# Optimization experiments

Measured on AMD Instinct MI355X. Metric: run time of the kernel, lower is better.

Reference implementation:

```python
import jax, jax.numpy as jnp
import numpy as np

EPS = 1e-12

def _l2norm(x):
    # F.normalize(p=2, dim=1) with eps clamp on the norm
    n = jnp.linalg.norm(x, axis=1, keepdims=True)
    return x / jnp.maximum(n, EPS)

def _xavier_uniform(key, shape, gain=1.414):
    fan_in, fan_out = shape[-1], shape[0]
    a = gain * np.sqrt(6.0 / (fan_in + fan_out))
    return jax.random.uniform(key, shape, jnp.float32, -a, a)

def setup_inputs() -> dict:
    NUM_ENT, NUM_REL, D, E, B = 100000, 500, 512, 150000, 4096
    key = jax.random.key(0)
    ks = jax.random.split(key, 12)
    heads = jax.random.randint(ks[0], (B, 1), 0, NUM_ENT)
    rels  = jax.random.randint(ks[1], (B, 1), 0, NUM_REL)
    tails = jax.random.randint(ks[2], (B, 1), 0, NUM_ENT)
    triples = jnp.concatenate([heads, rels, tails], axis=1)           # [B,3]
    node_list = jax.random.randint(ks[3], (2, E), 0, NUM_ENT)          # [2,E] (src,dst)
    edge_list = jax.random.randint(ks[4], (E,), 0, NUM_REL)            # [E] relation per edge
    return {
        "triples": triples,
        "node_list": node_list,
        "edge_list": edge_list,
        "ent_emb_init": jax.random.normal(ks[5], (NUM_ENT, D), jnp.float32),
        "rel_emb_init": jax.random.normal(ks[6], (NUM_REL, D), jnp.float32),
        "W_1": _xavier_uniform(ks[7], (D, D)),
        "W_a": _xavier_uniform(ks[8], (1, D)),
        "g_0": _xavier_uniform(ks[9], (1, D)),
        "W_E": _xavier_uniform(ks[10], (D, D)),
        "W_R": _xavier_uniform(ks[11], (D, D)),
    }

def reference(triples, node_list, edge_list, ent_emb_init, rel_emb_init,
              W_1, W_a, g_0, W_E, W_R):
    num_ent = ent_emb_init.shape[0]
    e0 = _l2norm(ent_emb_init)                      # normalized entity table [N,D]
    src, dst = node_list[0], node_list[1]
    h_i = e0[src]                                   # [E,D]
    h_j = e0[dst]                                   # [E,D]
    g_k = rel_emb_init[edge_list]                   # [E,D]

    # c_ijk = W_1 @ (h_j*g_k)^T  -> kept edge-major as [E,D]
    c = (h_j * g_k) @ W_1.T                         # [E,D]
    a = -jax.nn.leaky_relu((h_i * jnp.tanh(c)) @ W_a[0], 0.2)   # [E]
    c_base = (h_i * g_0) @ W_1.T                    # [E,D]
    a_base = -jax.nn.leaky_relu((h_i * jnp.tanh(c_base)) @ W_a[0], 0.2)  # [E]

    a_exp = jnp.exp(a)                              # [E]
    ab_exp = jnp.exp(a_base)                        # [E]

    # segment-softmax denominator: sum of edge exps per source node + baseline term
    a_exp_sum = jax.ops.segment_sum(a_exp[:, None], src, num_segments=num_ent)  # [N,1]
    # baseline exp depends only on src node -> duplicate scatter-set writes identical values
    ab_sorted = jnp.zeros_like(a_exp_sum).at[src].set(ab_exp[:, None])           # [N,1]
    denom = ab_sorted + a_exp_sum
    denom = jnp.where(denom == 0.0, EPS, denom)

    # weighted scatter-aggregate of messages (dropout omitted: eval-mode identity)
    ac = a_exp[:, None] * c                         # [E,D]
    ac_base = ab_exp[:, None] * c_base              # [E,D]
    a_new = jax.ops.segment_sum(ac, src, num_segments=num_ent)                   # [N,D]
    ab_new = jnp.zeros_like(a_new).at[src].set(ac_base)                          # [N,D]

    h_prime = jax.nn.elu((ab_new + a_new) / denom)  # [N,D]
    ent_new = _l2norm(e0 @ W_E + h_prime)           # [N,D]
    rel_new = rel_emb_init @ W_R                    # [R,D]

    head = ent_new[triples[:, 0]][:, None, :]       # [B,1,D]
    rel  = rel_new[triples[:, 1]][:, None, :]       # [B,1,D]
    tail = ent_new[triples[:, 2]][:, None, :]       # [B,1,D]
    return jnp.concatenate([head, rel, tail], axis=1)  # [B,3,D]
```

## Files before the change

kernel.cpp:

```cpp
#include <hip/hip_runtime.h>
#include <cmath>


#define DDIM 512
#define MAXM 65536
#define GBM 128
#define GBN 128

typedef __attribute__((ext_vector_type(8))) short short8;
typedef __attribute__((ext_vector_type(4))) float fv4;
typedef unsigned short u16;

__device__ __forceinline__ float elu1(float x) { return x > 0.f ? x : expm1f(x); }
__device__ __forceinline__ float sexp(float x) {
    float lr = x >= 0.f ? x : 0.2f * x;
    return expf(-lr);
}
__device__ __forceinline__ u16 f2bf(float x) {
    unsigned u = __float_as_uint(x);
    u += 0x7FFFu + ((u >> 16) & 1u);
    return (u16)(u >> 16);
}
__device__ __forceinline__ float bf2f(u16 h) {
    return __uint_as_float((unsigned)h << 16);
}
__device__ __forceinline__ void cvt8(const float* v, short8& h8, short8& l8) {
    #pragma unroll
    for (int i = 0; i < 8; i++) {
        u16 h = f2bf(v[i]);
        h8[i] = (short)h;
        l8[i] = (short)f2bf(v[i] - bf2f(h));
    }
}

__global__ __launch_bounds__(128)
void invnorm_sel_kernel(const float* __restrict__ emb, const int* __restrict__ slotNode,
                        const int* __restrict__ rowsL, const int* __restrict__ dstIdx,
                        const int* __restrict__ Mdev, int NS, float* __restrict__ invN)
{
    __shared__ float ws2[2];
    int total = NS + min(MAXM, *Mdev);
    int t = threadIdx.x;
    for (int q = blockIdx.x; q < total; q += gridDim.x) {
        int n = (q < NS) ? slotNode[q] : dstIdx[rowsL[q - NS]];
        float4 v = *(const float4*)(emb + (size_t)n * DDIM + t * 4);
        float s = v.x*v.x + v.y*v.y + v.z*v.z + v.w*v.w;
        #pragma unroll
        for (int off = 32; off > 0; off >>= 1) s += __shfl_down(s, off);
        if ((t & 63) == 0) ws2[t >> 6] = s;
        __syncthreads();
        if (t == 0) invN[n] = 1.f / fmaxf(sqrtf(ws2[0] + ws2[1]), 1e-12f);
        __syncthreads();
    }
}

__global__ __launch_bounds__(128)
void l2norm_kernel(float* __restrict__ data)
{
    int r = blockIdx.x, t = threadIdx.x;
    size_t o = (size_t)r * DDIM + t * 4;
    float4 v = *(const float4*)(data + o);
    float s = v.x*v.x + v.y*v.y + v.z*v.z + v.w*v.w;
    #pragma unroll
    for (int off = 32; off > 0; off >>= 1) s += __shfl_down(s, off);
    __shared__ float ws2[2];
    if ((t & 63) == 0) ws2[t >> 6] = s;
    __syncthreads();
    float inv = 1.f / fmaxf(sqrtf(ws2[0] + ws2[1]), 1e-12f);
    *(float4*)(data + o) = make_float4(v.x*inv, v.y*inv, v.z*inv, v.w*inv);
}

__global__ __launch_bounds__(256)
void transpose512_kernel(const float* __restrict__ in, float* __restrict__ out)
{
    __shared__ float tile[32][33];
    int bx = blockIdx.x & 15, by = blockIdx.x >> 4;
    int x = threadIdx.x & 31, y0 = (threadIdx.x >> 5) * 4;
    #pragma unroll
    for (int i = 0; i < 4; i++)
        tile[y0 + i][x] = in[(size_t)(by * 32 + y0 + i) * 512 + bx * 32 + x];
    __syncthreads();
    #pragma unroll
    for (int i = 0; i < 4; i++)
        out[(size_t)(bx * 32 + y0 + i) * 512 + by * 32 + x] = tile[x][y0 + i];
}

__global__ void hist_kernel(const int* __restrict__ src, int* __restrict__ cnt, int E)
{
    int e = blockIdx.x * 256 + threadIdx.x;
    if (e < E) atomicAdd(&cnt[src[e]], 1);
}

__global__ __launch_bounds__(1024)
void scan1_kernel(const int* __restrict__ in, int* __restrict__ out,
                  int* __restrict__ blockTot, int n)
{
    __shared__ int sh[1024];
    int t = threadIdx.x;
    int i = blockIdx.x * 1024 + t;
    int v = (i < n) ? in[i] : 0;
    sh[t] = v;
    __syncthreads();
    for (int off = 1; off < 1024; off <<= 1) {
        int x = (t >= off) ? sh[t - off] : 0;
        __syncthreads();
        sh[t] += x;
        __syncthreads();
    }
    if (i < n) out[i] = sh[t] - v;
    if (t == 1023) blockTot[blockIdx.x] = sh[1023];
}

__global__ __launch_bounds__(1024)
void scan2_kernel(const int* __restrict__ blockTot, int* __restrict__ blockOff,
                  int* __restrict__ outLast, int G)
{
    __shared__ int sh[1024];
    int t = threadIdx.x;
    int v = (t < G) ? blockTot[t] : 0;
    sh[t] = v;
    __syncthreads();
    for (int off = 1; off < 1024; off <<= 1) {
        int x = (t >= off) ? sh[t - off] : 0;
        __syncthreads();
        sh[t] += x;
        __syncthreads();
    }
    if (t < G) blockOff[t] = sh[t] - v;
    if (t == 1023) *outLast = sh[1023];
}

__global__ __launch_bounds__(1024)
void scan3_kernel(int* __restrict__ out, const int* __restrict__ blockOff, int n)
{
    int i = blockIdx.x * 1024 + threadIdx.x;
    if (i < n) out[i] += blockOff[blockIdx.x];
}

__global__ void bucket_kernel(const int* __restrict__ src, int* __restrict__ cursor,
                              int* __restrict__ edge_ids, int E)
{
    int e = blockIdx.x * 256 + threadIdx.x;
    if (e < E) { int p = atomicAdd(&cursor[src[e]], 1); edge_ids[p] = e; }
}

__global__ void slotdeg_kernel(const int* __restrict__ triples, const int* __restrict__ rowSt,
                               int* __restrict__ slotNode, int* __restrict__ deg, int NS)
{
    int r = blockIdx.x * 256 + threadIdx.x;
    if (r < NS) {
        int b = r >> 1, p = (r & 1) * 2;
        int n = triples[b * 3 + p];
        slotNode[r] = n;
        deg[r] = rowSt[n + 1] - rowSt[n];
    }
}

__global__ void fill_rows_kernel(const int* __restrict__ slotNode, const int* __restrict__ rowSt,
                                 const int* __restrict__ edgeIds, const int* __restrict__ slotOff,
                                 int* __restrict__ rows, int* __restrict__ srcL, int NS)
{
    int r = blockIdx.x * 256 + threadIdx.x;
    if (r >= NS) return;
    int n = slotNode[r];
    int gs = rowSt[n], d = rowSt[n + 1] - gs, mo = slotOff[r];
    for (int j = 0; j < d && mo + j < MAXM; j++) {
        rows[mo + j] = edgeIds[gs + j];
        srcL[mo + j] = n;
    }
}

__global__ __launch_bounds__(256)
void afrag_dense_kernel(const float* __restrict__ in, int rows,
                        u16* __restrict__ hi, u16* __restrict__ lo)
{
    int nt = ((rows + 127) >> 7) << 3;
    int wid = threadIdx.x >> 6, lane = threadIdx.x & 63;
    int l15 = lane & 15, seg = (lane >> 4) * 8;
    for (int rt = blockIdx.x * 4 + wid; rt < nt; rt += gridDim.x * 4) {
        int r = min(rt * 16 + l15, rows - 1);
        const float* p = in + (size_t)r * DDIM + seg;
        size_t base = (size_t)rt * 8192 + (size_t)lane * 8;
        #pragma unroll 4
        for (int kt = 0; kt < 16; kt++) {
            float4 x0 = *(const float4*)(p + kt * 32);
            float4 x1 = *(const float4*)(p + kt * 32 + 4);
            float v[8] = {x0.x, x0.y, x0.z, x0.w, x1.x, x1.y, x1.z, x1.w};
            short8 h8, l8; cvt8(v, h8, l8);
            *(short8*)(hi + base + (size_t)kt * 512) = h8;
            *(short8*)(lo + base + (size_t)kt * 512) = l8;
        }
    }
}

__global__ __launch_bounds__(256)
void afrag_edge_kernel(const float* __restrict__ entEmb, const float* __restrict__ invN,
                       const float* __restrict__ relEmb, const int* __restrict__ rowsL,
                       const int* __restrict__ dstIdx, const int* __restrict__ relIdx,
                       const int* __restrict__ Mdev,
                       u16* __restrict__ hi, u16* __restrict__ lo)
{
    int M = max(1, min(MAXM, *Mdev));
    int nt = ((M + 127) >> 7) << 3;
    int wid = threadIdx.x >> 6, lane = threadIdx.x & 63;
    int l15 = lane & 15, seg = (lane >> 4) * 8;
    for (int rt = blockIdx.x * 4 + wid; rt < nt; rt += gridDim.x * 4) {
        int m = min(rt * 16 + l15, M - 1);
        int e = rowsL[m];
        int dn = dstIdx[e], rl = relIdx[e];
        float sc = invN[dn];
        const float* ep = entEmb + (size_t)dn * DDIM + seg;
        const float* rp = relEmb + (size_t)rl * DDIM + seg;
        size_t base = (size_t)rt * 8192 + (size_t)lane * 8;
        #pragma unroll 4
        for (int kt = 0; kt < 16; kt++) {
            float4 x0 = *(const float4*)(ep + kt * 32);
            float4 x1 = *(const float4*)(ep + kt * 32 + 4);
            float4 y0 = *(const float4*)(rp + kt * 32);
            float4 y1 = *(const float4*)(rp + kt * 32 + 4);
            float v[8] = {sc*x0.x*y0.x, sc*x0.y*y0.y, sc*x0.z*y0.z, sc*x0.w*y0.w,
                          sc*x1.x*y1.x, sc*x1.y*y1.y, sc*x1.z*y1.z, sc*x1.w*y1.w};
            short8 h8, l8; cvt8(v, h8, l8);
            *(short8*)(hi + base + (size_t)kt * 512) = h8;
            *(short8*)(lo + base + (size_t)kt * 512) = l8;
        }
    }
}

__global__ __launch_bounds__(256)
void afrag_slot_kernel(const float* __restrict__ entEmb, const float* __restrict__ invN,
                       const float* __restrict__ g0, const int* __restrict__ slotNode,
                       int NS, u16* __restrict__ s1h, u16* __restrict__ s1l,
                       u16* __restrict__ s3h, u16* __restrict__ s3l)
{
    int nt = ((NS + 127) >> 7) << 3;
    int wid = threadIdx.x >> 6, lane = threadIdx.x & 63;
    int l15 = lane & 15, seg = (lane >> 4) * 8;
    for (int rt = blockIdx.x * 4 + wid; rt < nt; rt += gridDim.x * 4) {
        int r = min(rt * 16 + l15, NS - 1);
        int n = slotNode[r];
        float sc = invN[n];
        const float* ep = entEmb + (size_t)n * DDIM + seg;
        const float* gp = g0 + seg;
        size_t base = (size_t)rt * 8192 + (size_t)lane * 8;
        #pragma unroll 2
        for (int kt = 0; kt < 16; kt++) {
            float4 x0 = *(const float4*)(ep + kt * 32);
            float4 x1 = *(const float4*)(ep + kt * 32 + 4);
            float4 y0 = *(const float4*)(gp + kt * 32);
            float4 y1 = *(const float4*)(gp + kt * 32 + 4);
            float v3[8] = {sc*x0.x, sc*x0.y, sc*x0.z, sc*x0.w,
                           sc*x1.x, sc*x1.y, sc*x1.z, sc*x1.w};
            float v1[8] = {v3[0]*y0.x, v3[1]*y0.y, v3[2]*y0.z, v3[3]*y0.w,
                           v3[4]*y1.x, v3[5]*y1.y, v3[6]*y1.z, v3[7]*y1.w};
            short8 h8, l8;
            cvt8(v3, h8, l8);
            *(short8*)(s3h + base + (size_t)kt * 512) = h8;
            *(short8*)(s3l + base + (size_t)kt * 512) = l8;
            cvt8(v1, h8, l8);
            *(short8*)(s1h + base + (size_t)kt * 512) = h8;
            *(short8*)(s1l + base + (size_t)kt * 512) = l8;
        }
    }
}

template<int EPI, bool DEVM>
__global__ __launch_bounds__(256)
void gemm_frag_k(const u16* __restrict__ Ahi, const u16* __restrict__ Alo,
                 const u16* __restrict__ Bhi, const u16* __restrict__ Blo,
                 const float* __restrict__ entEmb, const float* __restrict__ invNorm,
                 const int* __restrict__ srcMap, const float* __restrict__ Wa,
                 float* __restrict__ scoreOut, const float* __restrict__ invDenom,
                 const float* __restrict__ Hadd, float* __restrict__ Cout,
                 int Mhost, const int* __restrict__ Mdev)
{
    int M = DEVM ? max(1, min(MAXM, *Mdev)) : Mhost;
    int lane = threadIdx.x & 63, wid = threadIdx.x >> 6;
    int waveM = wid >> 1, waveN = wid & 1;
    int quad = lane >> 4, l15 = lane & 15;
    int n0 = blockIdx.y * GBN;

    for (int mt = blockIdx.x; mt * GBM < M; mt += gridDim.x) {
        int m0 = mt * GBM;
        const u16 *aHp[4], *aLp[4], *bHp[4], *bLp[4];
        #pragma unroll
        for (int i = 0; i < 4; i++) {
            size_t rt = (size_t)(m0 >> 4) + waveM * 4 + i;
            aHp[i] = Ahi + rt * 8192 + (size_t)lane * 8;
            aLp[i] = Alo + rt * 8192 + (size_t)lane * 8;
            size_t ntb = (size_t)(n0 >> 4) + waveN * 4 + i;
            bHp[i] = Bhi + ntb * 8192 + (size_t)lane * 8;
            bLp[i] = Blo + ntb * 8192 + (size_t)lane * 8;
        }

        fv4 acc[4][4];
        #pragma unroll
        for (int i = 0; i < 4; i++)
            #pragma unroll
            for (int j = 0; j < 4; j++) acc[i][j] = fv4{0.f, 0.f, 0.f, 0.f};

        short8 aH[4], aL[4], bH[4], bL[4];
        #pragma unroll
        for (int i = 0; i < 4; i++) {
            aH[i] = *(const short8*)aHp[i];
            aL[i] = *(const short8*)aLp[i];
            bH[i] = *(const short8*)bHp[i];
            bL[i] = *(const short8*)bLp[i];
        }

        for (int kt = 0; kt < 16; kt++) {
            short8 nAH[4], nAL[4], nBH[4], nBL[4];
            if (kt < 15) {
                size_t o = (size_t)(kt + 1) * 512;
                #pragma unroll
                for (int i = 0; i < 4; i++) {
                    nAH[i] = *(const short8*)(aHp[i] + o);
                    nAL[i] = *(const short8*)(aLp[i] + o);
                    nBH[i] = *(const short8*)(bHp[i] + o);
                    nBL[i] = *(const short8*)(bLp[i] + o);
                }
            }
            #pragma unroll
            for (int i = 0; i < 4; i++)
                #pragma unroll
                for (int j = 0; j < 4; j++) {
                    acc[i][j] = __builtin_amdgcn_mfma_f32_16x16x32_bf16(aH[i], bH[j], acc[i][j], 0, 0, 0);
                    acc[i][j] = __builtin_amdgcn_mfma_f32_16x16x32_bf16(aH[i], bL[j], acc[i][j], 0, 0, 0);
                    acc[i][j] = __builtin_amdgcn_mfma_f32_16x16x32_bf16(aL[i], bH[j], acc[i][j], 0, 0, 0);
                }
            if (kt < 15) {
                #pragma unroll
                for (int i = 0; i < 4; i++) {
                    aH[i] = nAH[i]; aL[i] = nAL[i];
                    bH[i] = nBH[i]; bL[i] = nBL[i];
                }
            }
        }

        if (EPI == 1) {
            #pragma unroll
            for (int i = 0; i < 4; i++) {
                #pragma unroll
                for (int reg = 0; reg < 4; reg++) {
                    int gm = m0 + waveM * 64 + i * 16 + quad * 4 + reg;
                    bool valid = gm < M;
                    int gmc = valid ? gm : 0;
                    int srcn = srcMap[gmc];
                    float invs = invNorm[srcn];
                    float s = 0.f;
                    #pragma unroll
                    for (int j = 0; j < 4; j++) {
                        int col = n0 + waveN * 64 + j * 16 + l15;
                        float hv = entEmb[(size_t)srcn * DDIM + col];
                        float wv = Wa[col];
                        s += tanhf(acc[i][j][reg]) * hv * wv;
                    }
                    s *= invs;
                    s += __shfl_xor(s, 8); s += __shfl_xor(s, 4);
                    s += __shfl_xor(s, 2); s += __shfl_xor(s, 1);
                    if (l15 == 0 && valid) atomicAdd(scoreOut + gm, s);
                }
            }
        } else {
            #pragma unroll
            for (int i = 0; i < 4; i++) {
                #pragma unroll
                for (int reg = 0; reg < 4; reg++) {
                    int gm = m0 + waveM * 64 + i * 16 + quad * 4 + reg;
                    if (gm >= M) continue;
                    float idv = (EPI == 2) ? invDenom[gm] : 0.f;
                    #pragma unroll
                    for (int j = 0; j < 4; j++) {
                        int col = n0 + waveN * 64 + j * 16 + l15;
                        size_t o = (size_t)gm * DDIM + col;
                        float v = acc[i][j][reg];
                        if (EPI == 2) v = elu1(v * idv);
                        else if (EPI == 3) v += Hadd[o];
                        Cout[o] = v;
                    }
                }
            }
        }
    }
}

__global__ __launch_bounds__(128)
void build_p_kernel(const float* __restrict__ entEmb, const float* __restrict__ invNorm,
                    const float* __restrict__ relEmb, const float* __restrict__ g0,
                    const int* __restrict__ slotNode, const int* __restrict__ rowSt,
                    const int* __restrict__ edgeIds, const int* __restrict__ dstIdx,
                    const int* __restrict__ relIdx, const int* __restrict__ slotOff,
                    const float* __restrict__ scoreE, const float* __restrict__ scoreS,
                    float* __restrict__ P, float* __restrict__ invDenom)
{
    int r = blockIdx.x, t = threadIdx.x;
    int n = slotNode[r];
    int gs = rowSt[n], d = rowSt[n + 1] - gs;
    size_t po = (size_t)r * DDIM + t * 4;
    if (d == 0) {
        *(float4*)(P + po) = make_float4(0.f, 0.f, 0.f, 0.f);
        if (t == 0) invDenom[r] = 1.f;
        return;
    }
    int mo = slotOff[r];
    float ab = sexp(scoreS[r]);
    float sc = ab * invNorm[n];
    float4 ev = *(const float4*)(entEmb + (size_t)n * DDIM + t * 4);
    float4 gv = *(const float4*)(g0 + t * 4);
    float4 acc = make_float4(sc*ev.x*gv.x, sc*ev.y*gv.y, sc*ev.z*gv.z, sc*ev.w*gv.w);
    float denom = ab;
    for (int j = 0; j < d; j++) {
        if (mo + j >= MAXM) break;
        int e = edgeIds[gs + j];
        float ae = sexp(scoreE[mo + j]);
        int dn = dstIdx[e], rl = relIdx[e];
        float s = ae * invNorm[dn];
        float4 dv = *(const float4*)(entEmb + (size_t)dn * DDIM + t * 4);
        float4 rv = *(const float4*)(relEmb + (size_t)rl * DDIM + t * 4);
        acc.x = fmaf(s, dv.x*rv.x, acc.x);
        acc.y = fmaf(s, dv.y*rv.y, acc.y);
        acc.z = fmaf(s, dv.z*rv.z, acc.z);
        acc.w = fmaf(s, dv.w*rv.w, acc.w);
        denom += ae;
    }
    *(float4*)(P + po) = acc;
    if (t == 0) invDenom[r] = 1.f / denom;
}

__global__ __launch_bounds__(128)
void gather_out_kernel(const int* __restrict__ triples, const float* __restrict__ ENT,
                       const float* __restrict__ relnew, float* __restrict__ out)
{
    int r = blockIdx.x;
    int b = r / 3, j = r - b * 3;
    const float* srow;
    if (j == 1) srow = relnew + (size_t)triples[r] * DDIM;
    else        srow = ENT + (size_t)(b * 2 + (j == 2 ? 1 : 0)) * DDIM;
    int t = threadIdx.x * 4;
    *(float4*)(out + (size_t)r * DDIM + t) = *(const float4*)(srow + t);
}

extern "C" void kernel_launch(void* const* d_in, const int* in_sizes, int n_in,
                              void* d_out, int out_size, void* d_ws, size_t ws_size,
                              hipStream_t stream)
{
    const int*   triples = (const int*)  d_in[0];
    const int*   nodes   = (const int*)  d_in[1];
    const int*   edges   = (const int*)  d_in[2];
    const float* entEmb  = (const float*)d_in[3];
    const float* relEmb  = (const float*)d_in[4];
    const float* W1      = (const float*)d_in[5];
    const float* Wa      = (const float*)d_in[6];
    const float* g0      = (const float*)d_in[7];
    const float* WE      = (const float*)d_in[8];
    const float* WR      = (const float*)d_in[9];

    const int B  = in_sizes[0] / 3;
    const int E  = in_sizes[2];
    const int N  = in_sizes[3] / DDIM;
    const int R  = in_sizes[4] / DDIM;
    const int NS = 2 * B;
    const int* srcIdx = nodes;
    const int* dstIdx = nodes + E;

    char* ws = (char*)d_ws;
    size_t off = 0;
    auto carve = [&](size_t bytes) -> void* {
        void* p = ws + off;
        off = (off + bytes + 255) & ~(size_t)255;
        return p;
    };
    const int NS128 = ((NS + 127) / 128) * 128;
    const int R128  = ((R + 127) / 128) * 128;
    float* P        = (float*)carve((size_t)NS * DDIM * 4);
    float* H        = (float*)carve((size_t)NS * DDIM * 4);
    float* ENT      = (float*)carve((size_t)NS * DDIM * 4);
    float* relnew   = (float*)carve((size_t)R * DDIM * 4);
    float* WET      = (float*)carve((size_t)DDIM * DDIM * 4);
    float* WRT      = (float*)carve((size_t)DDIM * DDIM * 4);
    float* invNorm  = (float*)carve((size_t)N * 4);
    float* score_e  = (float*)carve((size_t)MAXM * 4);
    float* score_s  = (float*)carve((size_t)NS * 4);
    float* invDen   = (float*)carve((size_t)NS * 4);
    int*   cnt      = (int*)carve((size_t)N * 4);
    int*   rowSt    = (int*)carve((size_t)(N + 1) * 4);
    int*   cursor   = (int*)carve((size_t)N * 4);
    int*   edgeIds  = (int*)carve((size_t)E * 4);
    int*   slotNode = (int*)carve((size_t)NS * 4);
    int*   deg      = (int*)carve((size_t)NS * 4);
    int*   slotOff  = (int*)carve((size_t)(NS + 1) * 4);
    int*   rowsL    = (int*)carve((size_t)MAXM * 4);
    int*   srcL     = (int*)carve((size_t)MAXM * 4);
    int*   blockTot = (int*)carve((size_t)1024 * 4);
    int*   blockOff = (int*)carve((size_t)1024 * 4);
    u16* AeH = (u16*)carve((size_t)MAXM * DDIM * 2);
    u16* AeL = (u16*)carve((size_t)MAXM * DDIM * 2);
    u16* As1H = (u16*)carve((size_t)NS128 * DDIM * 2);
    u16* As1L = (u16*)carve((size_t)NS128 * DDIM * 2);
    u16* As3H = (u16*)carve((size_t)NS128 * DDIM * 2);
    u16* As3L = (u16*)carve((size_t)NS128 * DDIM * 2);
    u16* ApH = (u16*)carve((size_t)NS128 * DDIM * 2);
    u16* ApL = (u16*)carve((size_t)NS128 * DDIM * 2);
    u16* ArH = (u16*)carve((size_t)R128 * DDIM * 2);
    u16* ArL = (u16*)carve((size_t)R128 * DDIM * 2);
    u16* W1H = (u16*)carve((size_t)DDIM * DDIM * 2);
    u16* W1L = (u16*)carve((size_t)DDIM * DDIM * 2);
    u16* WEH = (u16*)carve((size_t)DDIM * DDIM * 2);
    u16* WEL = (u16*)carve((size_t)DDIM * DDIM * 2);
    u16* WRH = (u16*)carve((size_t)DDIM * DDIM * 2);
    u16* WRL = (u16*)carve((size_t)DDIM * DDIM * 2);
    (void)ws_size; (void)n_in; (void)out_size;

    auto scan = [&](const int* in, int* out, int n) {
        int G = (n + 1023) / 1024;
        scan1_kernel<<<G, 1024, 0, stream>>>(in, out, blockTot, n);
        scan2_kernel<<<1, 1024, 0, stream>>>(blockTot, blockOff, out + n, G);
        scan3_kernel<<<G, 1024, 0, stream>>>(out, blockOff, n);
    };

    hipMemsetAsync(cnt, 0, (size_t)N * 4, stream);
    hist_kernel<<<(E + 255) / 256, 256, 0, stream>>>(srcIdx, cnt, E);
    scan(cnt, rowSt, N);
    hipMemcpyAsync(cursor, rowSt, (size_t)N * 4, hipMemcpyDeviceToDevice, stream);
    bucket_kernel<<<(E + 255) / 256, 256, 0, stream>>>(srcIdx, cursor, edgeIds, E);

    slotdeg_kernel<<<(NS + 255) / 256, 256, 0, stream>>>(triples, rowSt, slotNode, deg, NS);
    scan(deg, slotOff, NS);
    fill_rows_kernel<<<(NS + 255) / 256, 256, 0, stream>>>(slotNode, rowSt, edgeIds,
                                                           slotOff, rowsL, srcL, NS);
    const int* Mdev = slotOff + NS;

    invnorm_sel_kernel<<<4096, 128, 0, stream>>>(entEmb, slotNode, rowsL, dstIdx,
                                                 Mdev, NS, invNorm);

    transpose512_kernel<<<256, 256, 0, stream>>>(WE, WET);
    transpose512_kernel<<<256, 256, 0, stream>>>(WR, WRT);
    afrag_dense_kernel<<<8, 256, 0, stream>>>(W1, DDIM, W1H, W1L);
    afrag_dense_kernel<<<8, 256, 0, stream>>>(WET, DDIM, WEH, WEL);
    afrag_dense_kernel<<<8, 256, 0, stream>>>(WRT, DDIM, WRH, WRL);

    afrag_edge_kernel<<<128, 256, 0, stream>>>(entEmb, invNorm, relEmb, rowsL,
                                               dstIdx, edges, Mdev, AeH, AeL);
    afrag_slot_kernel<<<128, 256, 0, stream>>>(entEmb, invNorm, g0, slotNode, NS,
                                               As1H, As1L, As3H, As3L);

    hipMemsetAsync(score_e, 0, (size_t)MAXM * 4, stream);
    hipMemsetAsync(score_s, 0, (size_t)NS * 4, stream);
    dim3 gEdge(128, DDIM / GBN);
    gemm_frag_k<1, true><<<gEdge, 256, 0, stream>>>(
        AeH, AeL, W1H, W1L, entEmb, invNorm, srcL, Wa,
        score_e, nullptr, nullptr, nullptr, 0, Mdev);
    dim3 gSlot((NS + GBM - 1) / GBM, DDIM / GBN);
    gemm_frag_k<1, false><<<gSlot, 256, 0, stream>>>(
        As1H, As1L, W1H, W1L, entEmb, invNorm, slotNode, Wa,
        score_s, nullptr, nullptr, nullptr, NS, nullptr);

    build_p_kernel<<<NS, 128, 0, stream>>>(entEmb, invNorm, relEmb, g0, slotNode,
                                           rowSt, edgeIds, dstIdx, edges, slotOff,
                                           score_e, score_s, P, invDen);

    afrag_dense_kernel<<<128, 256, 0, stream>>>(P, NS, ApH, ApL);
    gemm_frag_k<2, false><<<gSlot, 256, 0, stream>>>(
        ApH, ApL, W1H, W1L, entEmb, invNorm, nullptr, nullptr,
        nullptr, invDen, nullptr, H, NS, nullptr);

    gemm_frag_k<3, false><<<gSlot, 256, 0, stream>>>(
        As3H, As3L, WEH, WEL, entEmb, invNorm, nullptr, nullptr,
        nullptr, nullptr, H, ENT, NS, nullptr);
    l2norm_kernel<<<NS, 128, 0, stream>>>(ENT);

    afrag_dense_kernel<<<8, 256, 0, stream>>>(relEmb, R, ArH, ArL);
    dim3 gRel((R + GBM - 1) / GBM, DDIM / GBN);
    gemm_frag_k<0, false><<<gRel, 256, 0, stream>>>(
        ArH, ArL, WRH, WRL, entEmb, invNorm, nullptr, nullptr,
        nullptr, nullptr, nullptr, relnew, R, nullptr);

    gather_out_kernel<<<B * 3, 128, 0, stream>>>(triples, ENT, relnew, (float*)d_out);
}
```

Before: 592.0 us.

## Stage GEMM fragments through double-buffered LDS via direct global-to-LDS loads

Each of the four waves in a GEMM block now loads one operand class (A hi, A lo, B hi, B lo) straight into a double-buffered shared-memory tile using global_load_lds. All waves then read their fragments from LDS instead of each wave fetching its own fragments from global memory into registers. The aim is to remove duplicate global reads of shared A/B tiles across waves and to free registers used for prefetching. In exchange it adds two block barriers per k-step and 64KB of LDS per block, which may reduce occupancy. It also relies on vmcnt/barrier ordering for the async LDS loads being correct.

```diff
diff --git a/kernel.cpp b/kernel.cpp
--- a/kernel.cpp
+++ b/kernel.cpp
@@ -31,6 +31,12 @@
         h8[i] = (short)h;
         l8[i] = (short)f2bf(v[i] - bf2f(h));
     }
+}
+__device__ __forceinline__ void gld16(const void* g, void* l) {
+    __builtin_amdgcn_global_load_lds(
+        (const __attribute__((address_space(1))) unsigned int*)g,
+        (__attribute__((address_space(3))) unsigned int*)l,
+        16, 0, 0);
 }
 
 __global__ __launch_bounds__(128)
@@ -274,24 +280,21 @@
                  const float* __restrict__ Hadd, float* __restrict__ Cout,
                  int Mhost, const int* __restrict__ Mdev)
 {
+    __shared__ __align__(1024) u16 lds[2][32 * 512];
+
     int M = DEVM ? max(1, min(MAXM, *Mdev)) : Mhost;
     int lane = threadIdx.x & 63, wid = threadIdx.x >> 6;
     int waveM = wid >> 1, waveN = wid & 1;
     int quad = lane >> 4, l15 = lane & 15;
     int n0 = blockIdx.y * GBN;
 
+    const u16* gcls = (wid == 0) ? Ahi : (wid == 1) ? Alo : (wid == 2) ? Bhi : Blo;
+    int ldsChunk0 = wid * 8;
+
     for (int mt = blockIdx.x; mt * GBM < M; mt += gridDim.x) {
         int m0 = mt * GBM;
-        const u16 *aHp[4], *aLp[4], *bHp[4], *bLp[4];
-        #pragma unroll
-        for (int i = 0; i < 4; i++) {
-            size_t rt = (size_t)(m0 >> 4) + waveM * 4 + i;
-            aHp[i] = Ahi + rt * 8192 + (size_t)lane * 8;
-            aLp[i] = Alo + rt * 8192 + (size_t)lane * 8;
-            size_t ntb = (size_t)(n0 >> 4) + waveN * 4 + i;
-            bHp[i] = Bhi + ntb * 8192 + (size_t)lane * 8;
-            bLp[i] = Blo + ntb * 8192 + (size_t)lane * 8;
-        }
+        int rowBase = (wid < 2) ? (m0 >> 4) : (n0 >> 4);
+        const u16* src0 = gcls + (size_t)rowBase * 8192 + (size_t)lane * 8;
 
         fv4 acc[4][4];
         #pragma unroll
@@ -299,26 +302,28 @@
             #pragma unroll
             for (int j = 0; j < 4; j++) acc[i][j] = fv4{0.f, 0.f, 0.f, 0.f};
 
-        short8 aH[4], aL[4], bH[4], bL[4];
+        int cur = 0;
         #pragma unroll
-        for (int i = 0; i < 4; i++) {
-            aH[i] = *(const short8*)aHp[i];
-            aL[i] = *(const short8*)aLp[i];
-            bH[i] = *(const short8*)bHp[i];
-            bL[i] = *(const short8*)bLp[i];
-        }
+        for (int q = 0; q < 8; q++)
+            gld16(src0 + (size_t)q * 8192, &lds[0][(ldsChunk0 + q) * 512]);
+        __syncthreads();
 
         for (int kt = 0; kt < 16; kt++) {
-            short8 nAH[4], nAL[4], nBH[4], nBL[4];
             if (kt < 15) {
-                size_t o = (size_t)(kt + 1) * 512;
+                size_t go = (size_t)(kt + 1) * 512;
                 #pragma unroll
-                for (int i = 0; i < 4; i++) {
-                    nAH[i] = *(const short8*)(aHp[i] + o);
-                    nAL[i] = *(const short8*)(aLp[i] + o);
-                    nBH[i] = *(const short8*)(bHp[i] + o);
-                    nBL[i] = *(const short8*)(bLp[i] + o);
-                }
+                for (int q = 0; q < 8; q++)
+                    gld16(src0 + (size_t)q * 8192 + go,
+                          &lds[cur ^ 1][(ldsChunk0 + q) * 512]);
+            }
+            const u16* buf = &lds[cur][0];
+            short8 aH[4], aL[4], bH[4], bL[4];
+            #pragma unroll
+            for (int i = 0; i < 4; i++) {
+                aH[i] = *(const short8*)&buf[(waveM * 4 + i) * 512 + lane * 8];
+                aL[i] = *(const short8*)&buf[(8 + waveM * 4 + i) * 512 + lane * 8];
+                bH[i] = *(const short8*)&buf[(16 + waveN * 4 + i) * 512 + lane * 8];
+                bL[i] = *(const short8*)&buf[(24 + waveN * 4 + i) * 512 + lane * 8];
             }
             #pragma unroll
             for (int i = 0; i < 4; i++)
@@ -328,13 +333,8 @@
                     acc[i][j] = __builtin_amdgcn_mfma_f32_16x16x32_bf16(aH[i], bL[j], acc[i][j], 0, 0, 0);
                     acc[i][j] = __builtin_amdgcn_mfma_f32_16x16x32_bf16(aL[i], bH[j], acc[i][j], 0, 0, 0);
                 }
-            if (kt < 15) {
-                #pragma unroll
-                for (int i = 0; i < 4; i++) {
-                    aH[i] = nAH[i]; aL[i] = nAL[i];
-                    bH[i] = nBH[i]; bL[i] = nBL[i];
-                }
-            }
+            __syncthreads();
+            cur ^= 1;
         }
 
         if (EPI == 1) {
```

Measured after the change: 555.5 us. 6.2% less time.
